# Performance work log

Measured on AMD Instinct MI355X. Metric: run time of the kernel, lower is better.

Reference implementation:

```python
import jax, jax.numpy as jnp
import numpy as np

# ---- dims (match init_kwargs) ----
IMG = 128; PATCH = 16; GRID = IMG // PATCH; L = GRID * GRID  # 64 patches
D = 256            # embed_dim
EXP = 2; DIN = D * EXP          # d_inner = 512
DH = 64; H = DIN // DH          # 8 heads
G = 1; N = 64                   # n_groups, d_state
DCONV = 4
DEPTH = 2
NCLS = 1000
BATCH = 16
DINPROJ = 2 * DIN + 2 * G * N + H   # z | xBC | dt
CDIM = DIN + 2 * G * N              # conv channels
EPS = 1e-6

def _snake_indices():
    g = np.arange(L).reshape(GRID, GRID)
    g[1::2] = g[1::2, ::-1]
    return jnp.asarray(g.reshape(-1))

SNAKE = _snake_indices()

def rmsnorm(x, w):
    return x * jax.lax.rsqrt(jnp.mean(x * x, axis=-1, keepdims=True) + EPS) * w

def causal_depthwise_conv(x, w, b):
    # x: (B,L,C), w: (C,K) depthwise causal conv, then SiLU
    xp = jnp.pad(x, ((0, 0), (DCONV - 1, 0), (0, 0)))
    y = sum(xp[:, k:k + x.shape[1], :] * w[:, k] for k in range(DCONV))
    return jax.nn.silu(y + b)

def mamba_block(x, Win, cw, cb, dtb, Alog, Dp, gn, Wout):
    # Mamba-2/3 style selective scan block. x: (B,L,D)
    Bsz, Lx, _ = x.shape
    zxbcdt = x @ Win                                   # (B,L,DINPROJ)
    z   = zxbcdt[..., :DIN]
    xBC = zxbcdt[..., DIN:DIN + CDIM]
    dt  = jax.nn.softplus(zxbcdt[..., DIN + CDIM:] + dtb)   # (B,L,H)
    xBC = causal_depthwise_conv(xBC, cw, cb)
    xs = xBC[..., :DIN].reshape(Bsz, Lx, H, DH)
    Bm = xBC[..., DIN:DIN + G * N].reshape(Bsz, Lx, G, N)
    Cm = xBC[..., DIN + G * N:].reshape(Bsz, Lx, G, N)
    Bh = jnp.repeat(Bm, H // G, axis=2)                # (B,L,H,N)
    Ch = jnp.repeat(Cm, H // G, axis=2)
    decay = jnp.exp(dt * (-jnp.exp(Alog)))             # (B,L,H) in (0,1)
    dBx = jnp.einsum('blh,blhp,blhn->blhpn', dt, xs, Bh)
    def step(h, inp):
        d, u = inp
        h = d[..., None, None] * h + u
        return h, h
    _, hs = jax.lax.scan(step, jnp.zeros((Bsz, H, DH, N), x.dtype),
                         (jnp.moveaxis(decay, 1, 0), jnp.moveaxis(dBx, 1, 0)))
    hs = jnp.moveaxis(hs, 0, 1)                        # (B,L,H,DH,N)
    y = jnp.einsum('blhpn,blhn->blhp', hs, Ch) + Dp[None, None, :, None] * xs
    y = y.reshape(Bsz, Lx, DIN)
    y = rmsnorm(y * jax.nn.silu(z), gn)                # gated RMSNorm
    return y @ Wout                                    # (B,L,D)

def setup_inputs() -> dict:
    key = jax.random.key(0)
    ks = jax.random.split(key, 24)
    s_in = 1.0 / np.sqrt(D); s_out = 1.0 / np.sqrt(DIN)
    def blk(k):
        kk = jax.random.split(k, 8)
        return dict(
            Win=jax.random.normal(kk[0], (DEPTH, D, DINPROJ)) * s_in,
            cw=jax.random.normal(kk[1], (DEPTH, CDIM, DCONV)) * 0.3,
            cb=jnp.zeros((DEPTH, CDIM)),
            dtb=jax.random.normal(kk[2], (DEPTH, H)) * 0.1,
            Alog=jnp.log(jax.random.uniform(kk[3], (DEPTH, H), minval=1.0, maxval=16.0)),
            Dp=jnp.ones((DEPTH, H)),
            gn=jnp.ones((DEPTH, DIN)),
            Wout=jax.random.normal(kk[4], (DEPTH, DIN, D)) * s_out)
    f = blk(ks[0]); b = blk(ks[1])
    inp = {
        'x': jax.random.normal(ks[2], (BATCH, 3, IMG, IMG), dtype=jnp.float32),
        'patch_w': jax.random.normal(ks[3], (D, 3 * PATCH * PATCH)) * (1.0 / np.sqrt(3 * PATCH * PATCH)),
        'patch_b': jnp.zeros((D,)),
        'pos_embed': jax.random.normal(ks[4], (1, L, D)) * 0.02,
        'norms_w': jnp.ones((DEPTH, D)),
        'final_w': jnp.ones((D,)),
        'head_w': jax.random.normal(ks[5], (D, NCLS)) * (1.0 / np.sqrt(D)),
        'head_b': jnp.zeros((NCLS,)),
    }
    for nm, v in f.items():
        inp[nm + '_f'] = v
    for nm, v in b.items():
        inp[nm + '_b'] = v
    return inp

def reference(x, patch_w, patch_b, pos_embed, norms_w, final_w, head_w, head_b,
              Win_f, cw_f, cb_f, dtb_f, Alog_f, Dp_f, gn_f, Wout_f,
              Win_b, cw_b, cb_b, dtb_b, Alog_b, Dp_b, gn_b, Wout_b):
    Bsz = x.shape[0]
    # patch embed == Conv2d(kernel=stride=PATCH)
    p = x.reshape(Bsz, 3, GRID, PATCH, GRID, PATCH).transpose(0, 2, 4, 1, 3, 5)
    p = p.reshape(Bsz, L, 3 * PATCH * PATCH)
    t = p @ patch_w.T + patch_b                        # (B,L,D)
    t = t + pos_embed[0]
    t = t[:, SNAKE, :]                                 # snake scan order
    for i in range(DEPTH):
        nx = rmsnorm(t, norms_w[i])
        of = mamba_block(nx, Win_f[i], cw_f[i], cb_f[i], dtb_f[i], Alog_f[i], Dp_f[i], gn_f[i], Wout_f[i])
        ob = mamba_block(nx[:, ::-1, :], Win_b[i], cw_b[i], cb_b[i], dtb_b[i], Alog_b[i], Dp_b[i], gn_b[i], Wout_b[i])[:, ::-1, :]
        t = t + 0.5 * (of + ob)                        # drop_path_rate=0 -> identity
    t = rmsnorm(t, final_w)
    t = t.mean(axis=1)
    return t @ head_w + head_b
```

## Files before the change

### kernel.cpp

```cpp
#include <hip/hip_runtime.h>
#include <hip/hip_bf16.h>
#include <math.h>

#define IMG 128
#define PATCH 16
#define L 64
#define D 256
#define DIN 512
#define DH 64
#define H 8
#define NSTATE 64
#define DCONV 4
#define DEPTH 2
#define NCLS 1000
#define BATCH 16
#define DINPROJ 1160
#define CDIM 640
#define EPS 1e-6f
#define SLAB (BATCH * L * D)

typedef __attribute__((ext_vector_type(8))) short short8;
typedef __attribute__((ext_vector_type(4))) float f32x4;
typedef __attribute__((ext_vector_type(4))) unsigned short us4;
typedef unsigned short ushort_t;

__device__ __forceinline__ int snake_tok(int s){
    int r = s >> 3, c = s & 7;
    return (r & 1) ? (r * 8 + (7 - c)) : (r * 8 + c);
}
__device__ __forceinline__ float silu_f(float x){ return x / (1.f + expf(-x)); }
__device__ __forceinline__ float softplus_f(float x){ return x > 20.f ? x : log1pf(expf(x)); }
__device__ __forceinline__ ushort_t f2b(float f){
    __hip_bfloat16 h = __float2bfloat16(f);
    return *(ushort_t*)&h;
}

__global__ __launch_bounds__(256) void wconv_patch_k(
    const float* __restrict__ Win0, const float* __restrict__ Win1,
    const float* __restrict__ Wout0, const float* __restrict__ Wout1,
    ushort_t* __restrict__ wbuf,
    const float* __restrict__ x, const float* __restrict__ PW,
    float* __restrict__ partP)
{
    __shared__ __align__(16) unsigned char SM[20480];
    const int task = blockIdx.x;
    const int tid = threadIdx.x;
    if (task < 1696){
        float (*sm)[33] = (float(*)[33])SM;
        const float* src; ushort_t* dst; int R, C, ctiles, tile;
        if (task < 1184){
            int z = task / 296; tile = task - z * 296;
            src = (z & 1 ? Win1 : Win0) + (size_t)(z >> 1) * D * DINPROJ;
            dst = wbuf + (size_t)z * 296960;
            R = D; C = DINPROJ; ctiles = 37;
        } else {
            int k = task - 1184;
            int z = k >> 7; tile = k & 127;
            src = (z & 1 ? Wout1 : Wout0) + (size_t)(z >> 1) * DIN * D;
            dst = wbuf + 1187840 + (size_t)z * 131072;
            R = DIN; C = D; ctiles = 8;
        }
        int cx = tile % ctiles, ry = tile / ctiles;
        int c0 = cx * 32, r0 = ry * 32;
        int tx = tid & 31, ty = tid >> 5;
        #pragma unroll
        for (int k = 0; k < 4; ++k){
            int r = r0 + ty + 8 * k, c = c0 + tx;
            sm[ty + 8 * k][tx] = (c < C) ? src[(size_t)r * C + c] : 0.f;
        }
        __syncthreads();
        #pragma unroll
        for (int k = 0; k < 4; ++k){
            int dr = c0 + ty + 8 * k, dc = r0 + tx;
            if (dr < C) dst[(size_t)dr * R + dc] = f2b(sm[tx][ty + 8 * k]);
        }
        return;
    }
    ushort_t (*As)[64][40] = (ushort_t(*)[64][40])SM;
    ushort_t (*Bs)[64][40] = (ushort_t(*)[64][40])(SM + 10240);
    const int pt = task - 1696;
    const int xi = pt & 3, b = (pt >> 2) & 15, split = pt >> 6;
    const int n0 = xi * 64;
    const int kbase = split * 384;
    const int lrow = tid >> 2, lc8 = (tid & 3) * 8;
    const int tok = snake_tok(lrow), gy = tok >> 3, gx = tok & 7;
    const float* xb = x + (size_t)b * 3 * IMG * IMG;
    const int wave = tid >> 6, lane = tid & 63;
    const int wm = (wave >> 1) * 32, wn = (wave & 1) * 32;
    const int fro = lane & 15, fk = (lane >> 4) * 8;

    f32x4 acc[2][2];
    #pragma unroll
    for (int i = 0; i < 2; ++i)
        #pragma unroll
        for (int j = 0; j < 2; ++j) acc[i][j] = (f32x4){0.f,0.f,0.f,0.f};

    short8 areg, breg;
    auto gload = [&](int kk){
        int k = kk + lc8;
        int c = k >> 8, rem = k & 255, py = rem >> 4, px = rem & 15;
        const float* srcA = xb + ((size_t)c * IMG + gy * PATCH + py) * IMG + gx * PATCH + px;
        float4 a0 = *(const float4*)(srcA);
        float4 a1 = *(const float4*)(srcA + 4);
        ushort_t ta[8] = {f2b(a0.x),f2b(a0.y),f2b(a0.z),f2b(a0.w),
                          f2b(a1.x),f2b(a1.y),f2b(a1.z),f2b(a1.w)};
        areg = *(short8*)ta;
        const float* srcB = PW + (size_t)(n0 + lrow) * 768 + kk + lc8;
        float4 b0 = *(const float4*)(srcB);
        float4 b1 = *(const float4*)(srcB + 4);
        ushort_t tb[8] = {f2b(b0.x),f2b(b0.y),f2b(b0.z),f2b(b0.w),
                          f2b(b1.x),f2b(b1.y),f2b(b1.z),f2b(b1.w)};
        breg = *(short8*)tb;
    };
    auto sstore = [&](int buf){
        *(short8*)&As[buf][lrow][lc8] = areg;
        *(short8*)&Bs[buf][lrow][lc8] = breg;
    };

    const int nk = 12;
    gload(kbase); sstore(0);
    __syncthreads();
    for (int kt = 0; kt < nk; ++kt){
        const int buf = kt & 1;
        if (kt + 1 < nk) gload(kbase + (kt + 1) * 32);
        short8 af[2], bfr[2];
        af[0]  = *(const short8*)&As[buf][wm + fro][fk];
        af[1]  = *(const short8*)&As[buf][wm + 16 + fro][fk];
        bfr[0] = *(const short8*)&Bs[buf][wn + fro][fk];
        bfr[1] = *(const short8*)&Bs[buf][wn + 16 + fro][fk];
        #pragma unroll
        for (int i = 0; i < 2; ++i)
            #pragma unroll
            for (int j = 0; j < 2; ++j)
                acc[i][j] = __builtin_amdgcn_mfma_f32_16x16x32_bf16(af[i], bfr[j], acc[i][j], 0, 0, 0);
        if (kt + 1 < nk) sstore(buf ^ 1);
        __syncthreads();
    }
    float* Cp = partP + (size_t)split * SLAB;
    #pragma unroll
    for (int i = 0; i < 2; ++i){
        #pragma unroll
        for (int j = 0; j < 2; ++j){
            int col = n0 + wn + j * 16 + (lane & 15);
            #pragma unroll
            for (int r = 0; r < 4; ++r){
                int srow = wm + i * 16 + (lane >> 4) * 4 + r;
                Cp[(size_t)(b * 64 + srow) * D + col] = acc[i][j][r];
            }
        }
    }
}

__global__ __launch_bounds__(256) void gemm_in_k(
    const float* __restrict__ partP, const float* __restrict__ pb,
    const float* __restrict__ pos, const float* __restrict__ pO,
    const float* __restrict__ nw,
    const ushort_t* __restrict__ B0, const ushort_t* __restrict__ B1,
    const float* __restrict__ cw0, const float* __restrict__ cw1,
    const float* __restrict__ cb0, const float* __restrict__ cb1,
    const float* __restrict__ dtb0, const float* __restrict__ dtb1,
    const float* __restrict__ Al0, const float* __restrict__ Al1,
    float* __restrict__ zb0, float* __restrict__ zb1,
    float* __restrict__ xy0, float* __restrict__ xy1,
    float* __restrict__ bc0, float* __restrict__ bc1,
    float* __restrict__ dts0, float* __restrict__ dts1,
    float* __restrict__ cums0, float* __restrict__ cums1)
{
    __shared__ __align__(16) ushort_t As[64][264];
    __shared__ __align__(16) ushort_t Bs[2][64][40];
    __shared__ float Ctile[64][68];
    const int dir = blockIdx.z;
    const ushort_t* __restrict__ Bw = dir ? B1 : B0;
    const int tid = threadIdx.x;
    const int m0 = blockIdx.y * 64, n0 = blockIdx.x * 64;
    const int b = blockIdx.y;
    const int arow = tid >> 2;
    const int wave = tid >> 6, lane = tid & 63;
    const int wm = (wave >> 1) * 32, wn = (wave & 1) * 32;
    const int fro = lane & 15, fk = (lane >> 4) * 8;

    {
        const int row = m0 + arow;
        const int tokr = snake_tok(row & 63);
        float4 vr[16];
        float ss = 0.f;
        #pragma unroll
        for (int i = 0; i < 16; ++i){
            int c = (tid & 3) * 4 + i * 16;
            size_t o = (size_t)row * D + c;
            float4 p0 = *(const float4*)(partP + o);
            float4 p1 = *(const float4*)(partP + SLAB + o);
            float4 bb = *(const float4*)(pb + c);
            float4 ps = *(const float4*)(pos + (size_t)tokr * D + c);
            float4 v;
            v.x = p0.x + p1.x + bb.x + ps.x;
            v.y = p0.y + p1.y + bb.y + ps.y;
            v.z = p0.z + p1.z + bb.z + ps.z;
            v.w = p0.w + p1.w + bb.w + ps.w;
            if (pO){
                float4 o0 = *(const float4*)(pO + o);
                float4 o1 = *(const float4*)(pO + SLAB + o);
                float4 o2 = *(const float4*)(pO + 2 * SLAB + o);
                float4 o3 = *(const float4*)(pO + 3 * SLAB + o);
                v.x += 0.5f * ((o0.x + o1.x) + (o2.x + o3.x));
                v.y += 0.5f * ((o0.y + o1.y) + (o2.y + o3.y));
                v.z += 0.5f * ((o0.z + o1.z) + (o2.z + o3.z));
                v.w += 0.5f * ((o0.w + o1.w) + (o2.w + o3.w));
            }
            vr[i] = v;
            ss += v.x*v.x + v.y*v.y + v.z*v.z + v.w*v.w;
        }
        ss += __shfl_xor(ss, 1);
        ss += __shfl_xor(ss, 2);
        float sc = rsqrtf(ss * (1.f / (float)D) + EPS);
        #pragma unroll
        for (int i = 0; i < 16; ++i){
            int c = (tid & 3) * 4 + i * 16;
            float4 w = *(const float4*)(nw + c);
            float4 v = vr[i];
            us4 ov = {f2b(v.x*sc*w.x), f2b(v.y*sc*w.y), f2b(v.z*sc*w.z), f2b(v.w*sc*w.w)};
            *(us4*)&As[arow][c] = ov;
        }
    }
    const int lrow = tid >> 2, lc8 = (tid & 3) * 8;
    float4 breg;
    auto gloadB = [&](int kk){
        int gn = n0 + lrow;
        if (gn < DINPROJ) breg = *(const float4*)(Bw + (size_t)gn * D + kk + lc8);
        else breg = make_float4(0.f,0.f,0.f,0.f);
    };
    auto sstoreB = [&](int buf){ *(float4*)&Bs[buf][lrow][lc8] = breg; };

    f32x4 acc[2][2];
    #pragma unroll
    for (int i = 0; i < 2; ++i)
        #pragma unroll
        for (int j = 0; j < 2; ++j) acc[i][j] = (f32x4){0.f,0.f,0.f,0.f};

    gloadB(0); sstoreB(0);
    __syncthreads();
    const int nk = D / 32;
    for (int kt = 0; kt < nk; ++kt){
        const int buf = kt & 1;
        if (kt + 1 < nk) gloadB((kt + 1) * 32);
        short8 af[2], bfr[2];
        af[0]  = *(const short8*)&As[wm + fro][kt * 32 + fk];
        af[1]  = *(const short8*)&As[wm + 16 + fro][kt * 32 + fk];
        bfr[0] = *(const short8*)&Bs[buf][wn + fro][fk];
        bfr[1] = *(const short8*)&Bs[buf][wn + 16 + fro][fk];
        #pragma unroll
        for (int i = 0; i < 2; ++i)
            #pragma unroll
            for (int j = 0; j < 2; ++j)
                acc[i][j] = __builtin_amdgcn_mfma_f32_16x16x32_bf16(af[i], bfr[j], acc[i][j], 0, 0, 0);
        if (kt + 1 < nk) sstoreB(buf ^ 1);
        __syncthreads();
    }

    if (n0 < DIN){
        float* zb = dir ? zb1 : zb0;
        #pragma unroll
        for (int i = 0; i < 2; ++i){
            #pragma unroll
            for (int j = 0; j < 2; ++j){
                int col = n0 + wn + j * 16 + (lane & 15);
                #pragma unroll
                for (int r = 0; r < 4; ++r){
                    int row = m0 + wm + i * 16 + (lane >> 4) * 4 + r;
                    zb[(size_t)row * DIN + col] = acc[i][j][r];
                }
            }
        }
        return;
    }

    #pragma unroll
    for (int i = 0; i < 2; ++i){
        #pragma unroll
        for (int j = 0; j < 2; ++j){
            int lcol = wn + j * 16 + (lane & 15);
            #pragma unroll
            for (int r = 0; r < 4; ++r){
                int lr = wm + i * 16 + (lane >> 4) * 4 + r;
                Ctile[lr][lcol] = acc[i][j][r];
            }
        }
    }
    __syncthreads();

    if (blockIdx.x < 18){
        const float* cw = dir ? cw1 : cw0;
        const float* cb = dir ? cb1 : cb0;
        float* xy = dir ? xy1 : xy0;
        float* bc = dir ? bc1 : bc0;
        const int c = tid & 63;
        const int cc = n0 - DIN + c;
        const float w0 = cw[cc * DCONV + 0], w1 = cw[cc * DCONV + 1];
        const float w2 = cw[cc * DCONV + 2], w3 = cw[cc * DCONV + 3];
        const float bb = cb[cc];
        #pragma unroll
        for (int rep = 0; rep < 16; ++rep){
            int s = (tid >> 6) + rep * 4;
            float a = bb;
            {
                int sp = s - 3;
                if (sp >= 0) a += w0 * Ctile[dir ? 63 - sp : sp][c];
                sp = s - 2;
                if (sp >= 0) a += w1 * Ctile[dir ? 63 - sp : sp][c];
                sp = s - 1;
                if (sp >= 0) a += w2 * Ctile[dir ? 63 - sp : sp][c];
                a += w3 * Ctile[dir ? 63 - s : s][c];
            }
            float v = silu_f(a);
            if (cc < DIN) xy[(size_t)(b * 64 + s) * DIN + cc] = v;
            else          bc[(size_t)(b * 64 + s) * 128 + (cc - DIN)] = v;
        }
        return;
    }

    {
        const float* dtb = dir ? dtb1 : dtb0;
        const float* Al  = dir ? Al1  : Al0;
        float* dts  = dir ? dts1  : dts0;
        float* cums = dir ? cums1 : cums0;
        int s = tid & 63;
        int l = dir ? (63 - s) : s;
        #pragma unroll
        for (int rep = 0; rep < 2; ++rep){
            int h = (tid >> 6) + rep * 4;
            float raw = Ctile[l][h] + dtb[h];
            float dt = softplus_f(raw);
            float val = -expf(Al[h]) * dt;
            #pragma unroll
            for (int o = 1; o < 64; o <<= 1){
                float u = __shfl_up(val, o);
                if (s >= o) val += u;
            }
            dts[(size_t)(b * 64 + s) * H + h]  = dt;
            cums[(size_t)(b * 64 + s) * H + h] = val;
        }
    }
}

__global__ __launch_bounds__(512) void yscan2_k(
    const float* __restrict__ bc0, const float* __restrict__ bc1,
    const float* __restrict__ dts0, const float* __restrict__ dts1,
    const float* __restrict__ cums0, const float* __restrict__ cums1,
    const float* __restrict__ Dp0, const float* __restrict__ Dp1,
    const float* __restrict__ zb0, const float* __restrict__ zb1,
    float* __restrict__ xy0, float* __restrict__ xy1,
    float* __restrict__ ssq0, float* __restrict__ ssq1)
{
    __shared__ float Bc[64][65];
    __shared__ float CX[64][65];
    __shared__ float Am[64][65];
    __shared__ float cumS[64], dtS[64];
    __shared__ float ssqp[8][64];
    const int h = blockIdx.x, b = blockIdx.y, dir = blockIdx.z;
    const float* bc   = dir ? bc1   : bc0;
    const float* dts  = dir ? dts1  : dts0;
    const float* cums = dir ? cums1 : cums0;
    const float* Dp   = dir ? Dp1   : Dp0;
    const float* zb   = dir ? zb1   : zb0;
    float* xy  = dir ? xy1  : xy0;
    float* ssq = dir ? ssq1 : ssq0;
    const int t = threadIdx.x;

    if (t < 64){
        cumS[t] = cums[(size_t)(b * L + t) * H + h];
        dtS[t]  = dts[(size_t)(b * L + t) * H + h];
    }
    for (int i = t; i < 4096; i += 512){
        int s = i >> 6, n = i & 63;
        Bc[s][n] = bc[(size_t)(b * L + s) * 128 + n];
        CX[s][n] = bc[(size_t)(b * L + s) * 128 + 64 + n];
    }
    __syncthreads();
    for (int i = t; i < 4096; i += 512){
        int s = i >> 6, j = i & 63;
        float v = 0.f;
        if (j <= s){
            float acc = 0.f;
            #pragma unroll
            for (int n = 0; n < 64; ++n) acc += CX[s][n] * Bc[j][n];
            v = acc * expf(cumS[s] - cumS[j]) * dtS[j];
        }
        Am[s][j] = v;
    }
    __syncthreads();
    for (int i = t; i < 4096; i += 512){
        int j = i >> 6, pp = i & 63;
        CX[j][pp] = xy[(size_t)(b * L + j) * DIN + h * DH + pp];
    }
    __syncthreads();
    {
        const int s = t & 63, pg = t >> 6;
        const int l = dir ? (63 - s) : s;
        const size_t row = (size_t)(b * 64 + l);
        const float dp = Dp[h];
        float acc[8];
        #pragma unroll
        for (int pp = 0; pp < 8; ++pp) acc[pp] = dp * CX[s][pg * 8 + pp];
        #pragma unroll
        for (int j = 0; j < 64; ++j){
            float am = Am[s][j];
            #pragma unroll
            for (int pp = 0; pp < 8; ++pp)
                acc[pp] = fmaf(am, CX[j][pg * 8 + pp], acc[pp]);
        }
        const float* zr = zb + row * DIN + h * DH + pg * 8;
        float4 z0 = *(const float4*)(zr);
        float4 z1 = *(const float4*)(zr + 4);
        float zv[8] = {z0.x, z0.y, z0.z, z0.w, z1.x, z1.y, z1.z, z1.w};
        float g2 = 0.f;
        float gout[8];
        #pragma unroll
        for (int pp = 0; pp < 8; ++pp){
            float g = acc[pp] * silu_f(zv[pp]);
            gout[pp] = g;
            g2 += g * g;
        }
        ssqp[pg][s] = g2;
        float* dst = xy + row * DIN + h * DH + pg * 8;
        *(float4*)(dst)     = make_float4(gout[0], gout[1], gout[2], gout[3]);
        *(float4*)(dst + 4) = make_float4(gout[4], gout[5], gout[6], gout[7]);
    }
    __syncthreads();
    if (t < 64){
        int ll = dir ? (63 - t) : t;
        float v = 0.f;
        #pragma unroll
        for (int q = 0; q < 8; ++q) v += ssqp[q][t];
        ssq[(size_t)(b * 64 + ll) * H + h] = v;
    }
}

__global__ __launch_bounds__(256) void gemm_out_k(
    const float* __restrict__ G0, const float* __restrict__ G1,
    const float* __restrict__ ssq0, const float* __restrict__ ssq1,
    const float* __restrict__ gn0, const float* __restrict__ gn1,
    const ushort_t* __restrict__ B0, const ushort_t* __restrict__ B1,
    float* __restrict__ part)
{
    __shared__ __align__(16) ushort_t As[2][64][40];
    __shared__ __align__(16) ushort_t Bs[2][64][40];
    __shared__ float scl[64];
    const int tid = threadIdx.x;
    const int n0 = blockIdx.x * 64, m0 = blockIdx.y * 64;
    const int z = blockIdx.z;
    const int dir = z >> 1;
    const int kbase = (z & 1) * 256;
    const float* __restrict__ G   = dir ? G1   : G0;
    const float* __restrict__ ssq = dir ? ssq1 : ssq0;
    const float* __restrict__ gnw = dir ? gn1  : gn0;
    const ushort_t* __restrict__ B = dir ? B1 : B0;
    const int lrow = tid >> 2, lc8 = (tid & 3) * 8;
    const int wave = tid >> 6, lane = tid & 63;
    const int wm = (wave >> 1) * 32, wn = (wave & 1) * 32;
    const int fro = lane & 15, fk = (lane >> 4) * 8;

    if (tid < 64){
        const float* sr = ssq + (size_t)(m0 + tid) * H;
        float v = (sr[0] + sr[1]) + (sr[2] + sr[3]) + (sr[4] + sr[5]) + (sr[6] + sr[7]);
        scl[tid] = rsqrtf(v * (1.f / (float)DIN) + EPS);
    }
    __syncthreads();

    short8 areg; float4 breg;
    auto gload = [&](int kk){
        const float* src = G + (size_t)(m0 + lrow) * DIN + kk + lc8;
        float4 a0 = *(const float4*)(src);
        float4 a1 = *(const float4*)(src + 4);
        const float* gw = gnw + kk + lc8;
        float4 w0 = *(const float4*)(gw);
        float4 w1 = *(const float4*)(gw + 4);
        float sc = scl[lrow];
        ushort_t ta[8] = {f2b(a0.x*sc*w0.x), f2b(a0.y*sc*w0.y), f2b(a0.z*sc*w0.z), f2b(a0.w*sc*w0.w),
                          f2b(a1.x*sc*w1.x), f2b(a1.y*sc*w1.y), f2b(a1.z*sc*w1.z), f2b(a1.w*sc*w1.w)};
        areg = *(short8*)ta;
        breg = *(const float4*)(B + (size_t)(n0 + lrow) * DIN + kk + lc8);
    };
    auto sstore = [&](int buf){
        *(short8*)&As[buf][lrow][lc8] = areg;
        *(float4*)&Bs[buf][lrow][lc8] = breg;
    };

    f32x4 acc[2][2];
    #pragma unroll
    for (int i = 0; i < 2; ++i)
        #pragma unroll
        for (int j = 0; j < 2; ++j) acc[i][j] = (f32x4){0.f,0.f,0.f,0.f};

    const int nk = 8;
    gload(kbase); sstore(0);
    __syncthreads();
    for (int kt = 0; kt < nk; ++kt){
        const int buf = kt & 1;
        if (kt + 1 < nk) gload(kbase + (kt + 1) * 32);
        short8 af[2], bfr[2];
        af[0]  = *(const short8*)&As[buf][wm + fro][fk];
        af[1]  = *(const short8*)&As[buf][wm + 16 + fro][fk];
        bfr[0] = *(const short8*)&Bs[buf][wn + fro][fk];
        bfr[1] = *(const short8*)&Bs[buf][wn + 16 + fro][fk];
        #pragma unroll
        for (int i = 0; i < 2; ++i)
            #pragma unroll
            for (int j = 0; j < 2; ++j)
                acc[i][j] = __builtin_amdgcn_mfma_f32_16x16x32_bf16(af[i], bfr[j], acc[i][j], 0, 0, 0);
        if (kt + 1 < nk) sstore(buf ^ 1);
        __syncthreads();
    }
    float* Cp = part + (size_t)z * SLAB;
    #pragma unroll
    for (int i = 0; i < 2; ++i){
        #pragma unroll
        for (int j = 0; j < 2; ++j){
            int col = n0 + wn + j * 16 + (lane & 15);
            #pragma unroll
            for (int r = 0; r < 4; ++r){
                int row = m0 + wm + i * 16 + (lane >> 4) * 4 + r;
                Cp[(size_t)row * D + col] = acc[i][j][r];
            }
        }
    }
}

__global__ void finalmean_k(const float* __restrict__ partP, const float* __restrict__ pb,
                            const float* __restrict__ pos,
                            const float* __restrict__ pO0, const float* __restrict__ pO1,
                            const float* __restrict__ fw, float* __restrict__ tm8){
    __shared__ float sm4[4];
    int b = blockIdx.x, q = blockIdx.y;
    int d = threadIdx.x;
    float a = 0.f;
    for (int r = 0; r < 8; ++r){
        int row = b * 64 + q * 8 + r;
        int tokr = snake_tok(row & 63);
        size_t o = (size_t)row * D + d;
        float v = (partP[o] + partP[SLAB + o]) + pb[d] + pos[(size_t)tokr * D + d];
        v += 0.5f * ((pO0[o] + pO0[SLAB + o]) + (pO0[2 * SLAB + o] + pO0[3 * SLAB + o]));
        v += 0.5f * ((pO1[o] + pO1[SLAB + o]) + (pO1[2 * SLAB + o] + pO1[3 * SLAB + o]));
        float ssl = v * v;
        #pragma unroll
        for (int off = 32; off > 0; off >>= 1) ssl += __shfl_down(ssl, off);
        if ((threadIdx.x & 63) == 0) sm4[threadIdx.x >> 6] = ssl;
        __syncthreads();
        float ss = sm4[0] + sm4[1] + sm4[2] + sm4[3];
        __syncthreads();
        float sc = rsqrtf(ss / (float)D + EPS);
        a += v * sc;
    }
    tm8[(q * BATCH + b) * D + d] = a * (1.f / (float)L) * fw[d];
}

__global__ void head_k(const float* __restrict__ tm8, const float* __restrict__ hw,
                       const float* __restrict__ hb, float* __restrict__ out){
    __shared__ float trs[2][256];
    int i0 = blockIdx.x * 256;
    int mmin = i0 / NCLS;
    int t = threadIdx.x;
    #pragma unroll
    for (int mm = 0; mm < 2; ++mm){
        int m = mmin + mm;
        float v = 0.f;
        if (m < BATCH){
            #pragma unroll
            for (int q = 0; q < 8; ++q)
                v += tm8[(q * BATCH + m) * D + t];
        }
        trs[mm][t] = v;
    }
    __syncthreads();
    int i = i0 + t;
    if (i >= BATCH * NCLS) return;
    int m = i / NCLS, n = i - m * NCLS;
    const float* tr = trs[m - mmin];
    const float* hc = hw + n;
    float a0 = 0.f, a1 = 0.f, a2 = 0.f, a3 = 0.f;
    #pragma unroll 4
    for (int k = 0; k < D; k += 4){
        a0 = fmaf(tr[k],     hc[(size_t)k * NCLS],       a0);
        a1 = fmaf(tr[k + 1], hc[(size_t)(k + 1) * NCLS], a1);
        a2 = fmaf(tr[k + 2], hc[(size_t)(k + 2) * NCLS], a2);
        a3 = fmaf(tr[k + 3], hc[(size_t)(k + 3) * NCLS], a3);
    }
    out[i] = (a0 + a1) + (a2 + a3) + hb[n];
}

extern "C" void kernel_launch(void* const* d_in, const int* in_sizes, int n_in,
                              void* d_out, int out_size, void* d_ws, size_t ws_size,
                              hipStream_t stream){
    (void)in_sizes; (void)n_in; (void)out_size; (void)ws_size;
    const float* x       = (const float*)d_in[0];
    const float* patch_w = (const float*)d_in[1];
    const float* patch_b = (const float*)d_in[2];
    const float* pos     = (const float*)d_in[3];
    const float* norms_w = (const float*)d_in[4];
    const float* final_w = (const float*)d_in[5];
    const float* head_w  = (const float*)d_in[6];
    const float* head_b  = (const float*)d_in[7];
    const float* Win[2]  = {(const float*)d_in[8],  (const float*)d_in[16]};
    const float* cw[2]   = {(const float*)d_in[9],  (const float*)d_in[17]};
    const float* cb[2]   = {(const float*)d_in[10], (const float*)d_in[18]};
    const float* dtb[2]  = {(const float*)d_in[11], (const float*)d_in[19]};
    const float* Alog[2] = {(const float*)d_in[12], (const float*)d_in[20]};
    const float* Dp[2]   = {(const float*)d_in[13], (const float*)d_in[21]};
    const float* gn[2]   = {(const float*)d_in[14], (const float*)d_in[22]};
    const float* Wout[2] = {(const float*)d_in[15], (const float*)d_in[23]};

    float* ws = (float*)d_ws;
    float* tm8   = ws;
    float* zb0   = tm8   + 32768;
    float* zb1   = zb0   + 524288;
    float* xy0   = zb1   + 524288;
    float* xy1   = xy0   + 524288;
    float* bc0   = xy1   + 524288;
    float* bc1   = bc0   + 131072;
    float* dts0  = bc1   + 131072;
    float* dts1  = dts0  + 8192;
    float* cum0  = dts1  + 8192;
    float* cum1  = cum0  + 8192;
    float* ssq0  = cum1  + 8192;
    float* ssq1  = ssq0  + 8192;
    float* partP = ssq1  + 8192;
    float* partO0= partP + 524288;
    float* partO1= partO0+ 1048576;
    float* f32end = partO1 + 1048576;

    ushort_t* wbuf = (ushort_t*)f32end;
    ushort_t* win_bf  = wbuf;
    ushort_t* wout_bf = wbuf + 1187840;

    wconv_patch_k<<<1824, 256, 0, stream>>>(
        Win[0], Win[1], Wout[0], Wout[1], wbuf, x, patch_w, partP);

    float* partOs[2] = {partO0, partO1};
    for (int i = 0; i < DEPTH; ++i){
        const float* cw0  = cw[0]   + (size_t)i * CDIM * DCONV;
        const float* cw1  = cw[1]   + (size_t)i * CDIM * DCONV;
        const float* cb0  = cb[0]   + (size_t)i * CDIM;
        const float* cb1  = cb[1]   + (size_t)i * CDIM;
        const float* dtb0 = dtb[0]  + (size_t)i * H;
        const float* dtb1 = dtb[1]  + (size_t)i * H;
        const float* Al0  = Alog[0] + (size_t)i * H;
        const float* Al1  = Alog[1] + (size_t)i * H;
        const float* Dp0  = Dp[0]   + (size_t)i * H;
        const float* Dp1  = Dp[1]   + (size_t)i * H;
        const float* gn0  = gn[0]   + (size_t)i * DIN;
        const float* gn1  = gn[1]   + (size_t)i * DIN;
        const ushort_t* Wi0 = win_bf  + (size_t)(2 * i + 0) * 296960;
        const ushort_t* Wi1 = win_bf  + (size_t)(2 * i + 1) * 296960;
        const ushort_t* Wo0 = wout_bf + (size_t)(2 * i + 0) * 131072;
        const ushort_t* Wo1 = wout_bf + (size_t)(2 * i + 1) * 131072;
        const float* pO = (i == 0) ? nullptr : partO0;

        gemm_in_k<<<dim3(19, 16, 2), 256, 0, stream>>>(
            partP, patch_b, pos, pO, norms_w + i * D, Wi0, Wi1,
            cw0, cw1, cb0, cb1, dtb0, dtb1, Al0, Al1,
            zb0, zb1, xy0, xy1, bc0, bc1, dts0, dts1, cum0, cum1);
        yscan2_k<<<dim3(H, BATCH, 2), 512, 0, stream>>>(
            bc0, bc1, dts0, dts1, cum0, cum1, Dp0, Dp1, zb0, zb1,
            xy0, xy1, ssq0, ssq1);
        gemm_out_k<<<dim3(4, 16, 4), 256, 0, stream>>>(
            xy0, xy1, ssq0, ssq1, gn0, gn1, Wo0, Wo1, partOs[i]);
    }

    finalmean_k<<<dim3(BATCH, 8), 256, 0, stream>>>(
        partP, patch_b, pos, partO0, partO1, final_w, tm8);
    head_k<<<(BATCH * NCLS + 255) / 256, 256, 0, stream>>>(
        tm8, head_w, head_b, (float*)d_out);
}
```

Baseline: 140.6 us.

## Raise split-K in patch and out GEMMs, split scan by halves, add reduction kernels

The patch-embed GEMM goes from 2-way to 8-way split-K and the output GEMM from 2-way to 4-way per direction, which launches more blocks. The selective-scan kernel now splits each (head, batch) into two 32-row halves and writes gated output to a separate buffer instead of in place. Partial sums are folded into a residual stream by new small reduction kernels, so gemm_in reads a single pre-reduced tensor. The aim is better GPU occupancy for these small problems, at the cost of extra kernel launches and more partial-sum memory traffic.

```diff
diff --git a/kernel.cpp b/kernel.cpp
--- a/kernel.cpp
+++ b/kernel.cpp
@@ -81,7 +81,7 @@
     const int pt = task - 1696;
     const int xi = pt & 3, b = (pt >> 2) & 15, split = pt >> 6;
     const int n0 = xi * 64;
-    const int kbase = split * 384;
+    const int kbase = split * 96;
     const int lrow = tid >> 2, lc8 = (tid & 3) * 8;
     const int tok = snake_tok(lrow), gy = tok >> 3, gx = tok & 7;
     const float* xb = x + (size_t)b * 3 * IMG * IMG;
@@ -117,7 +117,7 @@
         *(short8*)&Bs[buf][lrow][lc8] = breg;
     };
 
-    const int nk = 12;
+    const int nk = 3;
     gload(kbase); sstore(0);
     __syncthreads();
     for (int kt = 0; kt < nk; ++kt){
@@ -151,10 +151,18 @@
     }
 }
 
+__global__ void patch_red_k(const float* __restrict__ part, const float* __restrict__ pb,
+                            const float* __restrict__ pos, float* __restrict__ t){
+    int i = blockIdx.x * 256 + threadIdx.x;
+    int d = i & (D - 1), s = (i >> 8) & (L - 1);
+    float v = 0.f;
+    #pragma unroll
+    for (int r = 0; r < 8; ++r) v += part[i + r * SLAB];
+    t[i] = v + pb[d] + pos[snake_tok(s) * D + d];
+}
+
 __global__ __launch_bounds__(256) void gemm_in_k(
-    const float* __restrict__ partP, const float* __restrict__ pb,
-    const float* __restrict__ pos, const float* __restrict__ pO,
-    const float* __restrict__ nw,
+    const float* __restrict__ T, const float* __restrict__ nw,
     const ushort_t* __restrict__ B0, const ushort_t* __restrict__ B1,
     const float* __restrict__ cw0, const float* __restrict__ cw1,
     const float* __restrict__ cb0, const float* __restrict__ cb1,
@@ -180,34 +188,12 @@
     const int fro = lane & 15, fk = (lane >> 4) * 8;
 
     {
-        const int row = m0 + arow;
-        const int tokr = snake_tok(row & 63);
-        float4 vr[16];
+        const float* src = T + (size_t)(m0 + arow) * D;
         float ss = 0.f;
         #pragma unroll
         for (int i = 0; i < 16; ++i){
             int c = (tid & 3) * 4 + i * 16;
-            size_t o = (size_t)row * D + c;
-            float4 p0 = *(const float4*)(partP + o);
-            float4 p1 = *(const float4*)(partP + SLAB + o);
-            float4 bb = *(const float4*)(pb + c);
-            float4 ps = *(const float4*)(pos + (size_t)tokr * D + c);
-            float4 v;
-            v.x = p0.x + p1.x + bb.x + ps.x;
-            v.y = p0.y + p1.y + bb.y + ps.y;
-            v.z = p0.z + p1.z + bb.z + ps.z;
-            v.w = p0.w + p1.w + bb.w + ps.w;
-            if (pO){
-                float4 o0 = *(const float4*)(pO + o);
-                float4 o1 = *(const float4*)(pO + SLAB + o);
-                float4 o2 = *(const float4*)(pO + 2 * SLAB + o);
-                float4 o3 = *(const float4*)(pO + 3 * SLAB + o);
-                v.x += 0.5f * ((o0.x + o1.x) + (o2.x + o3.x));
-                v.y += 0.5f * ((o0.y + o1.y) + (o2.y + o3.y));
-                v.z += 0.5f * ((o0.z + o1.z) + (o2.z + o3.z));
-                v.w += 0.5f * ((o0.w + o1.w) + (o2.w + o3.w));
-            }
-            vr[i] = v;
+            float4 v = *(const float4*)(src + c);
             ss += v.x*v.x + v.y*v.y + v.z*v.z + v.w*v.w;
         }
         ss += __shfl_xor(ss, 1);
@@ -216,10 +202,10 @@
         #pragma unroll
         for (int i = 0; i < 16; ++i){
             int c = (tid & 3) * 4 + i * 16;
+            float4 v = *(const float4*)(src + c);
             float4 w = *(const float4*)(nw + c);
-            float4 v = vr[i];
-            us4 ov = {f2b(v.x*sc*w.x), f2b(v.y*sc*w.y), f2b(v.z*sc*w.z), f2b(v.w*sc*w.w)};
-            *(us4*)&As[arow][c] = ov;
+            us4 o = {f2b(v.x*sc*w.x), f2b(v.y*sc*w.y), f2b(v.z*sc*w.z), f2b(v.w*sc*w.w)};
+            *(us4*)&As[arow][c] = o;
         }
     }
     const int lrow = tid >> 2, lc8 = (tid & 3) * 8;
@@ -342,27 +328,33 @@
     }
 }
 
-__global__ __launch_bounds__(512) void yscan2_k(
+__global__ __launch_bounds__(512) void yscan3_k(
     const float* __restrict__ bc0, const float* __restrict__ bc1,
     const float* __restrict__ dts0, const float* __restrict__ dts1,
     const float* __restrict__ cums0, const float* __restrict__ cums1,
     const float* __restrict__ Dp0, const float* __restrict__ Dp1,
     const float* __restrict__ zb0, const float* __restrict__ zb1,
-    float* __restrict__ xy0, float* __restrict__ xy1,
+    const float* __restrict__ xy0, const float* __restrict__ xy1,
+    float* __restrict__ gb0, float* __restrict__ gb1,
     float* __restrict__ ssq0, float* __restrict__ ssq1)
 {
     __shared__ float Bc[64][65];
-    __shared__ float CX[64][65];
-    __shared__ float Am[64][65];
+    __shared__ float Xs[64][65];
+    __shared__ float Cc[32][65];
+    __shared__ float Am[32][65];
     __shared__ float cumS[64], dtS[64];
-    __shared__ float ssqp[8][64];
-    const int h = blockIdx.x, b = blockIdx.y, dir = blockIdx.z;
+    __shared__ float ssqp[16][32];
+    const int h = blockIdx.x, b = blockIdx.y;
+    const int zz = blockIdx.z;
+    const int dir = zz >> 1, half = zz & 1;
+    const int s0 = half * 32;
     const float* bc   = dir ? bc1   : bc0;
     const float* dts  = dir ? dts1  : dts0;
     const float* cums = dir ? cums1 : cums0;
     const float* Dp   = dir ? Dp1   : Dp0;
     const float* zb   = dir ? zb1   : zb0;
-    float* xy  = dir ? xy1  : xy0;
+    const float* xy   = dir ? xy1   : xy0;
+    float* gb  = dir ? gb1  : gb0;
     float* ssq = dir ? ssq1 : ssq0;
     const int t = threadIdx.x;
 
@@ -373,64 +365,63 @@
     for (int i = t; i < 4096; i += 512){
         int s = i >> 6, n = i & 63;
         Bc[s][n] = bc[(size_t)(b * L + s) * 128 + n];
-        CX[s][n] = bc[(size_t)(b * L + s) * 128 + 64 + n];
-    }
-    __syncthreads();
-    for (int i = t; i < 4096; i += 512){
-        int s = i >> 6, j = i & 63;
+        Xs[s][n] = xy[(size_t)(b * L + s) * DIN + h * DH + n];
+    }
+    for (int i = t; i < 2048; i += 512){
+        int sl = i >> 6, n = i & 63;
+        Cc[sl][n] = bc[(size_t)(b * L + s0 + sl) * 128 + 64 + n];
+    }
+    __syncthreads();
+    for (int i = t; i < 2048; i += 512){
+        int sl = i >> 6, j = i & 63;
+        int s = s0 + sl;
         float v = 0.f;
         if (j <= s){
             float acc = 0.f;
             #pragma unroll
-            for (int n = 0; n < 64; ++n) acc += CX[s][n] * Bc[j][n];
+            for (int n = 0; n < 64; ++n) acc += Cc[sl][n] * Bc[j][n];
             v = acc * expf(cumS[s] - cumS[j]) * dtS[j];
         }
-        Am[s][j] = v;
-    }
-    __syncthreads();
-    for (int i = t; i < 4096; i += 512){
-        int j = i >> 6, pp = i & 63;
-        CX[j][pp] = xy[(size_t)(b * L + j) * DIN + h * DH + pp];
+        Am[sl][j] = v;
     }
     __syncthreads();
     {
-        const int s = t & 63, pg = t >> 6;
+        const int sl = t & 31, pg = t >> 5;
+        const int s = s0 + sl;
         const int l = dir ? (63 - s) : s;
         const size_t row = (size_t)(b * 64 + l);
         const float dp = Dp[h];
-        float acc[8];
-        #pragma unroll
-        for (int pp = 0; pp < 8; ++pp) acc[pp] = dp * CX[s][pg * 8 + pp];
+        float acc[4];
+        #pragma unroll
+        for (int pp = 0; pp < 4; ++pp) acc[pp] = dp * Xs[s][pg * 4 + pp];
         #pragma unroll
         for (int j = 0; j < 64; ++j){
-            float am = Am[s][j];
-            #pragma unroll
-            for (int pp = 0; pp < 8; ++pp)
-                acc[pp] = fmaf(am, CX[j][pg * 8 + pp], acc[pp]);
-        }
-        const float* zr = zb + row * DIN + h * DH + pg * 8;
-        float4 z0 = *(const float4*)(zr);
-        float4 z1 = *(const float4*)(zr + 4);
-        float zv[8] = {z0.x, z0.y, z0.z, z0.w, z1.x, z1.y, z1.z, z1.w};
+            float am = Am[sl][j];
+            #pragma unroll
+            for (int pp = 0; pp < 4; ++pp)
+                acc[pp] = fmaf(am, Xs[j][pg * 4 + pp], acc[pp]);
+        }
+        float4 z4 = *(const float4*)(zb + row * DIN + h * DH + pg * 4);
+        float zv[4] = {z4.x, z4.y, z4.z, z4.w};
         float g2 = 0.f;
-        float gout[8];
-        #pragma unroll
-        for (int pp = 0; pp < 8; ++pp){
+        float gout[4];
+        #pragma unroll
+        for (int pp = 0; pp < 4; ++pp){
             float g = acc[pp] * silu_f(zv[pp]);
             gout[pp] = g;
             g2 += g * g;
         }
-        ssqp[pg][s] = g2;
-        float* dst = xy + row * DIN + h * DH + pg * 8;
-        *(float4*)(dst)     = make_float4(gout[0], gout[1], gout[2], gout[3]);
-        *(float4*)(dst + 4) = make_float4(gout[4], gout[5], gout[6], gout[7]);
-    }
-    __syncthreads();
-    if (t < 64){
-        int ll = dir ? (63 - t) : t;
+        ssqp[pg][sl] = g2;
+        *(float4*)(gb + row * DIN + h * DH + pg * 4) =
+            make_float4(gout[0], gout[1], gout[2], gout[3]);
+    }
+    __syncthreads();
+    if (t < 32){
+        int s = s0 + t;
+        int ll = dir ? (63 - s) : s;
         float v = 0.f;
         #pragma unroll
-        for (int q = 0; q < 8; ++q) v += ssqp[q][t];
+        for (int q = 0; q < 16; ++q) v += ssqp[q][t];
         ssq[(size_t)(b * 64 + ll) * H + h] = v;
     }
 }
@@ -448,8 +439,8 @@
     const int tid = threadIdx.x;
     const int n0 = blockIdx.x * 64, m0 = blockIdx.y * 64;
     const int z = blockIdx.z;
-    const int dir = z >> 1;
-    const int kbase = (z & 1) * 256;
+    const int dir = z >> 2;
+    const int kbase = (z & 3) * 128;
     const float* __restrict__ G   = dir ? G1   : G0;
     const float* __restrict__ ssq = dir ? ssq1 : ssq0;
     const float* __restrict__ gnw = dir ? gn1  : gn0;
@@ -491,7 +482,7 @@
         #pragma unroll
         for (int j = 0; j < 2; ++j) acc[i][j] = (f32x4){0.f,0.f,0.f,0.f};
 
-    const int nk = 8;
+    const int nk = 4;
     gload(kbase); sstore(0);
     __syncthreads();
     for (int kt = 0; kt < nk; ++kt){
@@ -525,9 +516,15 @@
     }
 }
 
-__global__ void finalmean_k(const float* __restrict__ partP, const float* __restrict__ pb,
-                            const float* __restrict__ pos,
-                            const float* __restrict__ pO0, const float* __restrict__ pO1,
+__global__ void out_red_k(const float* __restrict__ part, float* __restrict__ t){
+    int i = blockIdx.x * 256 + threadIdx.x;
+    float v = 0.f;
+    #pragma unroll
+    for (int r = 0; r < 8; ++r) v += part[i + r * SLAB];
+    t[i] += 0.5f * v;
+}
+
+__global__ void finalmean_k(const float* __restrict__ T, const float* __restrict__ part,
                             const float* __restrict__ fw, float* __restrict__ tm8){
     __shared__ float sm4[4];
     int b = blockIdx.x, q = blockIdx.y;
@@ -535,11 +532,11 @@
     float a = 0.f;
     for (int r = 0; r < 8; ++r){
         int row = b * 64 + q * 8 + r;
-        int tokr = snake_tok(row & 63);
         size_t o = (size_t)row * D + d;
-        float v = (partP[o] + partP[SLAB + o]) + pb[d] + pos[(size_t)tokr * D + d];
-        v += 0.5f * ((pO0[o] + pO0[SLAB + o]) + (pO0[2 * SLAB + o] + pO0[3 * SLAB + o]));
-        v += 0.5f * ((pO1[o] + pO1[SLAB + o]) + (pO1[2 * SLAB + o] + pO1[3 * SLAB + o]));
+        float pv = 0.f;
+        #pragma unroll
+        for (int u = 0; u < 8; ++u) pv += part[o + (size_t)u * SLAB];
+        float v = T[o] + 0.5f * pv;
         float ssl = v * v;
         #pragma unroll
         for (int off = 32; off > 0; off >>= 1) ssl += __shfl_down(ssl, off);
@@ -609,12 +606,15 @@
     const float* Wout[2] = {(const float*)d_in[15], (const float*)d_in[23]};
 
     float* ws = (float*)d_ws;
-    float* tm8   = ws;
+    float* t     = ws;
+    float* tm8   = t     + 262144;
     float* zb0   = tm8   + 32768;
     float* zb1   = zb0   + 524288;
     float* xy0   = zb1   + 524288;
     float* xy1   = xy0   + 524288;
-    float* bc0   = xy1   + 524288;
+    float* gb0   = xy1   + 524288;
+    float* gb1   = gb0   + 524288;
+    float* bc0   = gb1   + 524288;
     float* bc1   = bc0   + 131072;
     float* dts0  = bc1   + 131072;
     float* dts1  = dts0  + 8192;
@@ -623,18 +623,19 @@
     float* ssq0  = cum1  + 8192;
     float* ssq1  = ssq0  + 8192;
     float* partP = ssq1  + 8192;
-    float* partO0= partP + 524288;
-    float* partO1= partO0+ 1048576;
-    float* f32end = partO1 + 1048576;
+    float* partO = partP + 2097152;
+    float* f32end = partO + 2097152;
 
     ushort_t* wbuf = (ushort_t*)f32end;
     ushort_t* win_bf  = wbuf;
     ushort_t* wout_bf = wbuf + 1187840;
 
-    wconv_patch_k<<<1824, 256, 0, stream>>>(
+    const int BL = BATCH * L;
+
+    wconv_patch_k<<<2208, 256, 0, stream>>>(
         Win[0], Win[1], Wout[0], Wout[1], wbuf, x, patch_w, partP);
-
-    float* partOs[2] = {partO0, partO1};
+    patch_red_k<<<BL, 256, 0, stream>>>(partP, patch_b, pos, t);
+
     for (int i = 0; i < DEPTH; ++i){
         const float* cw0  = cw[0]   + (size_t)i * CDIM * DCONV;
         const float* cw1  = cw[1]   + (size_t)i * CDIM * DCONV;
@@ -652,21 +653,20 @@
         const ushort_t* Wi1 = win_bf  + (size_t)(2 * i + 1) * 296960;
         const ushort_t* Wo0 = wout_bf + (size_t)(2 * i + 0) * 131072;
         const ushort_t* Wo1 = wout_bf + (size_t)(2 * i + 1) * 131072;
-        const float* pO = (i == 0) ? nullptr : partO0;
 
         gemm_in_k<<<dim3(19, 16, 2), 256, 0, stream>>>(
-            partP, patch_b, pos, pO, norms_w + i * D, Wi0, Wi1,
-            cw0, cw1, cb0, cb1, dtb0, dtb1, Al0, Al1,
-            zb0, zb1, xy0, xy1, bc0, bc1, dts0, dts1, cum0, cum1);
-        yscan2_k<<<dim3(H, BATCH, 2), 512, 0, stream>>>(
+            t, norms_w + i * D, Wi0, Wi1, cw0, cw1, cb0, cb1, dtb0, dtb1,
+            Al0, Al1, zb0, zb1, xy0, xy1, bc0, bc1, dts0, dts1, cum0, cum1);
+        yscan3_k<<<dim3(H, BATCH, 4), 512, 0, stream>>>(
             bc0, bc1, dts0, dts1, cum0, cum1, Dp0, Dp1, zb0, zb1,
-            xy0, xy1, ssq0, ssq1);
-        gemm_out_k<<<dim3(4, 16, 4), 256, 0, stream>>>(
-            xy0, xy1, ssq0, ssq1, gn0, gn1, Wo0, Wo1, partOs[i]);
-    }
-
-    finalmean_k<<<dim3(BATCH, 8), 256, 0, stream>>>(
-        partP, patch_b, pos, partO0, partO1, final_w, tm8);
+            xy0, xy1, gb0, gb1, ssq0, ssq1);
+        gemm_out_k<<<dim3(4, 16, 8), 256, 0, stream>>>(
+            gb0, gb1, ssq0, ssq1, gn0, gn1, Wo0, Wo1, partO);
+        if (i == 0)
+            out_red_k<<<BL, 256, 0, stream>>>(partO, t);
+    }
+
+    finalmean_k<<<dim3(BATCH, 8), 256, 0, stream>>>(t, partO, final_w, tm8);
     head_k<<<(BATCH * NCLS + 255) / 256, 256, 0, stream>>>(
         tm8, head_w, head_b, (float*)d_out);
 }
```

Result: faster. 129.2 us (-8.1%).
